# Optimization experiments

Measured on AMD Instinct MI355X. Metric: run time of the kernel, lower is better.

The kernel has to match this reference:

```python
import jax, jax.numpy as jnp
import numpy as np

N = 50000      # nodes
E = 800000     # edges
F_IN = 128     # input feature dim (OGBN-MAG paper features)
H = 4          # attention heads
HID = 64       # hidden_dim (per-head out channels)
HC = H * HID   # 256, concat output width
NC = 349       # num_classes
BN_EPS = 1e-5


def setup_inputs() -> dict:
    key = jax.random.key(0)
    ks = jax.random.split(key, 32)
    s = 0.05
    inp = {
        "x": jax.random.normal(ks[0], (N, F_IN), dtype=jnp.float32),
        "edge_index": jax.random.randint(ks[1], (2, E), 0, N, dtype=jnp.int64),
    }
    dins = [F_IN, HC]
    i = 2
    for l in range(2):
        d = dins[l]
        inp[f"ws{l}"] = jax.random.normal(ks[i], (d, HC), jnp.float32) * s; i += 1
        inp[f"wd{l}"] = jax.random.normal(ks[i], (d, HC), jnp.float32) * s; i += 1
        inp[f"atts{l}"] = jax.random.normal(ks[i], (H, HID), jnp.float32) * s; i += 1
        inp[f"attd{l}"] = jax.random.normal(ks[i], (H, HID), jnp.float32) * s; i += 1
        inp[f"bg{l}"] = jnp.zeros((HC,), jnp.float32); i += 1
        inp[f"lw{l}"] = jax.random.normal(ks[i], (d, HC), jnp.float32) * s; i += 1
        inp[f"lb{l}"] = jnp.zeros((HC,), jnp.float32); i += 1
        inp[f"g{l}"] = jnp.ones((HC,), jnp.float32); i += 1
        inp[f"b{l}"] = jnp.zeros((HC,), jnp.float32); i += 1
    inp["fcw"] = jax.random.normal(ks[i], (HC, NC), jnp.float32) * s
    inp["fcb"] = jnp.zeros((NC,), jnp.float32)
    return inp


def _gat(x, src, dst, ws, wd, atts, attd, bias):
    # PyG GATConv: separate src/dst projections, per-edge additive attention,
    # softmax over incoming edges of each dst node, scatter-add aggregation.
    n = x.shape[0]
    xs = (x @ ws).reshape(n, H, HID)            # [N,H,C] source messages
    xd = (x @ wd).reshape(n, H, HID)
    a_s = jnp.einsum("nhc,hc->nh", xs, atts)    # alpha_src
    a_d = jnp.einsum("nhc,hc->nh", xd, attd)    # alpha_dst
    e = jax.nn.leaky_relu(a_s[src] + a_d[dst], 0.2)   # [E,H]
    m = jax.ops.segment_max(e, dst, num_segments=n)   # segment-softmax (stable)
    ex = jnp.exp(e - m[dst])
    den = jax.ops.segment_sum(ex, dst, num_segments=n)
    w = ex / (den[dst] + 1e-16)                 # [E,H]
    out = jax.ops.segment_sum(xs[src] * w[:, :, None], dst, num_segments=n)
    return out.reshape(n, HC) + bias


def _bn(h, gamma, beta):
    # training-mode BatchNorm1d: batch statistics over nodes, biased variance
    mu = jnp.mean(h, axis=0)
    var = jnp.mean(jnp.square(h - mu), axis=0)
    return (h - mu) * jax.lax.rsqrt(var + BN_EPS) * gamma + beta


def reference(x, edge_index, ws0, wd0, atts0, attd0, bg0, lw0, lb0, g0, b0,
              ws1, wd1, atts1, attd1, bg1, lw1, lb1, g1, b1, fcw, fcb):
    src, dst = edge_index[0], edge_index[1]
    h = _gat(x, src, dst, ws0, wd0, atts0, attd0, bg0) + x @ lw0 + lb0
    h = jax.nn.relu(_bn(h, g0, b0))
    h = _gat(h, src, dst, ws1, wd1, atts1, attd1, bg1) + h @ lw1 + lb1
    h = jax.nn.relu(_bn(h, g1, b1))
    return h @ fcw + fcb
```

## Files before the change

### kernel.cpp

```cpp
#include <hip/hip_runtime.h>
#include <hip/hip_bf16.h>
#include <math.h>

#define N_NODES 50000
#define MPAD 50048
#define N_EDGES 800000
#define HCH 256
#define NHEAD 4
#define HIDC 64
#define NCLS 349
#define F_IN 128

typedef short short8 __attribute__((ext_vector_type(8)));
typedef float floatx4 __attribute__((ext_vector_type(4)));

__global__ void k_detect(const unsigned* ei, int* flag) {
    if (blockIdx.x == 0 && threadIdx.x == 0) {
        int i64 = 1;
        for (int e = 0; e < 64; e++)
            if (ei[2 * e + 1] != 0u) { i64 = 0; break; }
        *flag = i64;
    }
}

__device__ __forceinline__ void edge_sd(const int* ei, int e, int i64, int& s, int& d) {
    if (i64) {
        const long long* p = (const long long*)ei;
        s = (int)p[e]; d = (int)p[N_EDGES + e];
    } else {
        s = ei[e]; d = ei[N_EDGES + e];
    }
}

__global__ void k_deg(const int* ei, const int* flag, int* deg) {
    int e = blockIdx.x * 256 + threadIdx.x;
    if (e >= N_EDGES) return;
    int s, d; edge_sd(ei, e, *flag, s, d);
    atomicAdd(&deg[d], 1);
}

__global__ __launch_bounds__(256) void k_scan1(const int* __restrict__ deg,
                                               int* __restrict__ rowptr,
                                               int* __restrict__ bsum) {
    __shared__ int sd[256];
    int t = threadIdx.x;
    int base = blockIdx.x * 1024 + t * 4;
    int d0 = 0, d1 = 0, d2 = 0, d3 = 0;
    if (base + 3 < N_NODES) {
        int4 v = *(const int4*)(deg + base);
        d0 = v.x; d1 = v.y; d2 = v.z; d3 = v.w;
    } else {
        if (base + 0 < N_NODES) d0 = deg[base + 0];
        if (base + 1 < N_NODES) d1 = deg[base + 1];
        if (base + 2 < N_NODES) d2 = deg[base + 2];
        if (base + 3 < N_NODES) d3 = deg[base + 3];
    }
    int ts = d0 + d1 + d2 + d3;
    sd[t] = ts;
    __syncthreads();
    #pragma unroll
    for (int off = 1; off < 256; off <<= 1) {
        int v = (t >= off) ? sd[t - off] : 0;
        __syncthreads();
        sd[t] += v;
        __syncthreads();
    }
    int excl = (t == 0) ? 0 : sd[t - 1];
    if (base + 0 < N_NODES) rowptr[base + 0] = excl;
    if (base + 1 < N_NODES) rowptr[base + 1] = excl + d0;
    if (base + 2 < N_NODES) rowptr[base + 2] = excl + d0 + d1;
    if (base + 3 < N_NODES) rowptr[base + 3] = excl + d0 + d1 + d2;
    if (t == 255) bsum[blockIdx.x] = sd[255];
}

__global__ void k_scan2(int* __restrict__ bsum, int nb, int* __restrict__ rowptr) {
    int lane = threadIdx.x;
    int orig = (lane < nb) ? bsum[lane] : 0;
    int v = orig;
    #pragma unroll
    for (int off = 1; off < 64; off <<= 1) {
        int tv = __shfl_up(v, off, 64);
        if (lane >= off) v += tv;
    }
    if (lane < nb) bsum[lane] = v - orig;
    if (lane == 0) rowptr[N_NODES] = N_EDGES;
}

__global__ __launch_bounds__(256) void k_scan3(int* __restrict__ rowptr,
                                               const int* __restrict__ bsum) {
    int base = blockIdx.x * 1024 + threadIdx.x * 4;
    int off = bsum[blockIdx.x];
    if (base + 3 < N_NODES) {
        int4 v = *(int4*)(rowptr + base);
        v.x += off; v.y += off; v.z += off; v.w += off;
        *(int4*)(rowptr + base) = v;
    } else {
        for (int j = 0; j < 4; j++)
            if (base + j < N_NODES) rowptr[base + j] += off;
    }
}

__global__ void k_fill(const int* ei, const int* flag, const int* __restrict__ rowptr,
                       int* cursor, int* __restrict__ esrc) {
    int e = blockIdx.x * 256 + threadIdx.x;
    if (e >= N_EDGES) return;
    int s, d; edge_sd(ei, e, *flag, s, d);
    int pos = atomicAdd(&cursor[d], 1);
    esrc[rowptr[d] + pos] = s;
}

__global__ void k_wtilde(const float* __restrict__ ws, const float* __restrict__ wd,
                         const float* __restrict__ atts, const float* __restrict__ attd,
                         float* __restrict__ wt, int d) {
    int id = blockIdx.x * 256 + threadIdx.x;
    if (id >= d * 8) return;
    int j = id & 7, k = id >> 3;
    const float* w = (j < 4) ? ws : wd;
    const float* at = (j < 4) ? atts : attd;
    int h = j & 3;
    float s = 0.f;
    for (int c = 0; c < HIDC; c++) s += w[k * HCH + h * HIDC + c] * at[h * HIDC + c];
    wt[k * 8 + j] = s;
}

__device__ __forceinline__ unsigned short b16(float v) {
    __hip_bfloat16 t = __float2bfloat16(v);
    return *(unsigned short*)&t;
}

__device__ __forceinline__ float bfu(unsigned short u) {
    unsigned v = (unsigned)u << 16;
    return __builtin_bit_cast(float, v);
}

__device__ __forceinline__ void bsplit(float v, unsigned short& h, unsigned short& l) {
    __hip_bfloat16 bh = __float2bfloat16(v);
    float hv = __bfloat162float(bh);
    __hip_bfloat16 bl = __float2bfloat16(v - hv);
    h = *(unsigned short*)&bh;
    l = *(unsigned short*)&bl;
}

__global__ __launch_bounds__(256) void k_xcast(const float* __restrict__ x,
                                               unsigned short* __restrict__ xb) {
    size_t tot = (size_t)N_NODES * 128 / 4;
    for (size_t i = (size_t)blockIdx.x * 256 + threadIdx.x; i < tot;
         i += (size_t)gridDim.x * 256) {
        float4 v = *(const float4*)(x + i * 4);
        ushort4 o = {b16(v.x), b16(v.y), b16(v.z), b16(v.w)};
        *(ushort4*)(xb + i * 4) = o;
    }
}

__global__ void k_wcat_t(const float* __restrict__ ws, const float* __restrict__ lw,
                         const float* __restrict__ wtil, int K,
                         unsigned short* __restrict__ Bh, unsigned short* __restrict__ Bl) {
    int id = blockIdx.x * 256 + threadIdx.x;
    if (id >= 640 * K) return;
    int c = id / K, k = id % K;
    float v;
    if (c < 256) v = ws[(size_t)k * 256 + c];
    else if (c < 512) v = lw[(size_t)k * 256 + (c - 256)];
    else if (c < 520) v = wtil[(size_t)k * 8 + (c - 512)];
    else v = 0.f;
    unsigned short h, l;
    bsplit(v, h, l);
    Bh[(size_t)c * K + k] = h;
    Bl[(size_t)c * K + k] = l;
}

__global__ void k_fcw_t(const float* __restrict__ fcw, int K,
                        unsigned short* __restrict__ Bh, unsigned short* __restrict__ Bl) {
    int id = blockIdx.x * 256 + threadIdx.x;
    if (id >= 384 * K) return;
    int c = id / K, k = id % K;
    float v = (c < NCLS) ? fcw[(size_t)k * NCLS + c] : 0.f;
    unsigned short h, l;
    bsplit(v, h, l);
    Bh[(size_t)c * K + k] = h;
    Bl[(size_t)c * K + k] = l;
}

__device__ __forceinline__ void gload16(const void* g, void* l) {
    __builtin_amdgcn_global_load_lds(
        (const __attribute__((address_space(1))) void*)g,
        (__attribute__((address_space(3))) void*)l, 16, 0, 0);
}

__global__ __launch_bounds__(256) void k_gemm2(
    const unsigned short* __restrict__ Ab,
    const unsigned short* __restrict__ Bh, const unsigned short* __restrict__ Bl,
    float* __restrict__ C, int ldc, __hip_bfloat16* __restrict__ xsb,
    __hip_bfloat16* __restrict__ linbb, float* __restrict__ aout,
    const float* __restrict__ bias, int M, int K, int Nc) {
    __shared__ unsigned short sA[4096];
    __shared__ unsigned short sBh[4096];
    __shared__ unsigned short sBl[4096];
    int tid = threadIdx.x;
    int lane = tid & 63, wave = tid >> 6;
    int wm = wave >> 1, wn = wave & 1;
    int row0 = blockIdx.x * 128, col0 = blockIdx.y * 128;

    int rowq[2], kcq[2];
    #pragma unroll
    for (int q = 0; q < 2; q++) {
        int lds16 = wave * 128 + q * 64 + lane;
        int line = lds16 >> 3;
        int slot0 = (lds16 & 7) ^ (line & 7);
        rowq[q] = (line << 1) | (slot0 >> 2);
        kcq[q] = slot0 & 3;
    }
    int kc = lane >> 4, fr = lane & 15;
    int offA[4], offB[4];
    #pragma unroll
    for (int i = 0; i < 4; i++) {
        int ar = wm * 64 + i * 16 + fr;
        int ln = ar >> 1;
        int sl = (((ar & 1) << 2) | kc) ^ (ln & 7);
        offA[i] = ln * 128 + sl * 16;
        int bc = wn * 64 + i * 16 + fr;
        ln = bc >> 1;
        sl = (((bc & 1) << 2) | kc) ^ (ln & 7);
        offB[i] = ln * 128 + sl * 16;
    }

    floatx4 acc[4][4] = {};
    for (int k0 = 0; k0 < K; k0 += 32) {
        #pragma unroll
        for (int q = 0; q < 2; q++) {
            int lb = wave * 2048 + q * 1024;
            gload16(Ab + (size_t)(row0 + rowq[q]) * K + k0 + kcq[q] * 8, (char*)sA + lb);
            gload16(Bh + (size_t)(col0 + rowq[q]) * K + k0 + kcq[q] * 8, (char*)sBh + lb);
            gload16(Bl + (size_t)(col0 + rowq[q]) * K + k0 + kcq[q] * 8, (char*)sBl + lb);
        }
        __syncthreads();
        short8 fah[4], fbh[4], fbl[4];
        #pragma unroll
        for (int i = 0; i < 4; i++) {
            fah[i] = *(const short8*)((const char*)sA + offA[i]);
            fbh[i] = *(const short8*)((const char*)sBh + offB[i]);
            fbl[i] = *(const short8*)((const char*)sBl + offB[i]);
        }
        #pragma unroll
        for (int i = 0; i < 4; i++)
            #pragma unroll
            for (int j = 0; j < 4; j++) {
                acc[i][j] = __builtin_amdgcn_mfma_f32_16x16x32_bf16(fah[i], fbh[j], acc[i][j], 0, 0, 0);
                acc[i][j] = __builtin_amdgcn_mfma_f32_16x16x32_bf16(fah[i], fbl[j], acc[i][j], 0, 0, 0);
            }
        __syncthreads();
    }
    #pragma unroll
    for (int i = 0; i < 4; i++) {
        #pragma unroll
        for (int j = 0; j < 4; j++) {
            int c = col0 + wn * 64 + j * 16 + fr;
            if (c >= Nc) continue;
            float bv = bias ? bias[c] : 0.f;
            #pragma unroll
            for (int q = 0; q < 4; q++) {
                int r = row0 + wm * 64 + i * 16 + (lane >> 4) * 4 + q;
                if (r >= M) continue;
                float val = acc[i][j][q] + bv;
                if (C) C[(size_t)r * ldc + c] = val;
                else if (c < 256) xsb[(size_t)r * 256 + c] = __float2bfloat16(val);
                else if (c < 512) linbb[(size_t)r * 256 + (c - 256)] = __float2bfloat16(val);
                else aout[(size_t)r * 8 + (c - 512)] = val;
            }
        }
    }
}

#define LEAKY_EXP(vv) __expf(((vv) > 0.f) ? (vv) : 0.2f * (vv))

__global__ __launch_bounds__(256) void k_agg(
    const __hip_bfloat16* __restrict__ xsb,
    const __hip_bfloat16* __restrict__ linb, const float* __restrict__ a,
    const int* __restrict__ rowptr, const int* __restrict__ esrc,
    const float* __restrict__ bg, const float* __restrict__ lb,
    __hip_bfloat16* __restrict__ hout) {
    int wave = threadIdx.x >> 6;
    int lane = threadIdx.x & 63;
    int n = blockIdx.x * 4 + wave;
    if (n >= N_NODES) return;
    int h = lane >> 4;
    int c0 = lane * 4;
    float ad = a[(size_t)n * 8 + 4 + h];
    int beg = rowptr[n], end = rowptr[n + 1];
    float a0 = 0.f, a1 = 0.f, a2 = 0.f, a3 = 0.f, dsum = 0.f;
    int k = beg;
    for (; k + 8 <= end; k += 8) {
        int s[8];
        #pragma unroll
        for (int u = 0; u < 8; u++) s[u] = esrc[k + u];
        ushort4 m[8];
        #pragma unroll
        for (int u = 0; u < 8; u++)
            m[u] = *(const ushort4*)(xsb + (size_t)s[u] * 256 + c0);
        float av[8];
        #pragma unroll
        for (int u = 0; u < 8; u++) av[u] = a[(size_t)s[u] * 8 + h];
        #pragma unroll
        for (int u = 0; u < 8; u++) {
            float ev = LEAKY_EXP(av[u] + ad);
            a0 += bfu(m[u].x) * ev;
            a1 += bfu(m[u].y) * ev;
            a2 += bfu(m[u].z) * ev;
            a3 += bfu(m[u].w) * ev;
            dsum += ev;
        }
    }
    for (; k < end; k++) {
        int s = esrc[k];
        ushort4 m = *(const ushort4*)(xsb + (size_t)s * 256 + c0);
        float ev = LEAKY_EXP(a[(size_t)s * 8 + h] + ad);
        a0 += bfu(m.x) * ev;
        a1 += bfu(m.y) * ev;
        a2 += bfu(m.z) * ev;
        a3 += bfu(m.w) * ev;
        dsum += ev;
    }
    float inv = 1.f / (dsum + 1e-16f);
    float4 bgv = *(const float4*)(bg + c0);
    float4 lbv = *(const float4*)(lb + c0);
    ushort4 lnv = *(const ushort4*)(linb + (size_t)n * 256 + c0);
    ushort4 o;
    o.x = b16(a0 * inv + bgv.x + bfu(lnv.x) + lbv.x);
    o.y = b16(a1 * inv + bgv.y + bfu(lnv.y) + lbv.y);
    o.z = b16(a2 * inv + bgv.z + bfu(lnv.z) + lbv.z);
    o.w = b16(a3 * inv + bgv.w + bfu(lnv.w) + lbv.w);
    *(ushort4*)(hout + (size_t)n * 256 + c0) = o;
}

__global__ void k_bnstats(const __hip_bfloat16* __restrict__ hb,
                          float* __restrict__ bnsum, float* __restrict__ bnsq) {
    int c = threadIdx.x;
    float s = 0.f, q = 0.f;
    for (int r = blockIdx.x; r < N_NODES; r += gridDim.x) {
        float v = __bfloat162float(hb[(size_t)r * 256 + c]);
        s += v; q += v * v;
    }
    atomicAdd(&bnsum[c], s);
    atomicAdd(&bnsq[c], q);
}

__global__ __launch_bounds__(256) void k_bnapply(
    const __hip_bfloat16* __restrict__ hb, __hip_bfloat16* __restrict__ hpost,
    const float* __restrict__ bnsum, const float* __restrict__ bnsq,
    const float* __restrict__ g, const float* __restrict__ b) {
    __shared__ float sA[256], sB[256];
    int t = threadIdx.x;
    {
        float m = bnsum[t] / (float)N_NODES;
        float v = bnsq[t] / (float)N_NODES - m * m;
        float rs = rsqrtf(v + 1e-5f) * g[t];
        sA[t] = rs;
        sB[t] = b[t] - m * rs;
    }
    __syncthreads();
    size_t tot = (size_t)N_NODES * 256;
    for (size_t i = (size_t)blockIdx.x * 256 + t; i < tot;
         i += (size_t)gridDim.x * 256) {
        int c = (int)(i & 255);
        float v = __bfloat162float(hb[i]) * sA[c] + sB[c];
        v = v > 0.f ? v : 0.f;
        hpost[i] = __float2bfloat16(v);
    }
}

extern "C" void kernel_launch(void* const* d_in, const int* in_sizes, int n_in,
                              void* d_out, int out_size, void* d_ws, size_t ws_size,
                              hipStream_t stream) {
    const float* x     = (const float*)d_in[0];
    const int*   ei    = (const int*)d_in[1];
    const float* ws0   = (const float*)d_in[2];
    const float* wd0   = (const float*)d_in[3];
    const float* atts0 = (const float*)d_in[4];
    const float* attd0 = (const float*)d_in[5];
    const float* bg0   = (const float*)d_in[6];
    const float* lw0   = (const float*)d_in[7];
    const float* lb0   = (const float*)d_in[8];
    const float* g0    = (const float*)d_in[9];
    const float* b0    = (const float*)d_in[10];
    const float* ws1   = (const float*)d_in[11];
    const float* wd1   = (const float*)d_in[12];
    const float* atts1 = (const float*)d_in[13];
    const float* attd1 = (const float*)d_in[14];
    const float* bg1   = (const float*)d_in[15];
    const float* lw1   = (const float*)d_in[16];
    const float* lb1   = (const float*)d_in[17];
    const float* g1    = (const float*)d_in[18];
    const float* b1    = (const float*)d_in[19];
    const float* fcw   = (const float*)d_in[20];
    const float* fcb   = (const float*)d_in[21];
    float* out = (float*)d_out;

    char* p = (char*)d_ws;
    auto alloc = [&](size_t bytes) -> char* {
        char* r = p;
        p += (bytes + 255) & ~(size_t)255;
        return r;
    };
    __hip_bfloat16* xsb   = (__hip_bfloat16*)alloc((size_t)N_NODES * 256 * 2);
    __hip_bfloat16* linb  = (__hip_bfloat16*)alloc((size_t)N_NODES * 256 * 2);
    __hip_bfloat16* hb    = (__hip_bfloat16*)alloc((size_t)N_NODES * 256 * 2);
    __hip_bfloat16* hpost = (__hip_bfloat16*)alloc((size_t)MPAD * 256 * 2);
    unsigned short* xb    = (unsigned short*)alloc((size_t)MPAD * 128 * 2);
    float* a      = (float*)alloc((size_t)N_NODES * 8 * 4);
    int*   esrc   = (int*)alloc((size_t)N_EDGES * 4);
    int*   rowptr = (int*)alloc((size_t)(N_NODES + 1) * 4);
    int*   bsum   = (int*)alloc(64 * 4);
    unsigned short* w0h = (unsigned short*)alloc((size_t)640 * 128 * 2);
    unsigned short* w0l = (unsigned short*)alloc((size_t)640 * 128 * 2);
    unsigned short* w1h = (unsigned short*)alloc((size_t)640 * 256 * 2);
    unsigned short* w1l = (unsigned short*)alloc((size_t)640 * 256 * 2);
    unsigned short* fch = (unsigned short*)alloc((size_t)384 * 256 * 2);
    unsigned short* fcl = (unsigned short*)alloc((size_t)384 * 256 * 2);
    float* wtil   = (float*)alloc((size_t)256 * 8 * 4);
    int*   flag   = (int*)alloc(256);
    size_t zr_bytes = (size_t)N_NODES * 4 * 2 + 4 * 256 * 4;
    char* zbase = alloc(zr_bytes);
    int*   deg    = (int*)zbase;
    int*   cursor = deg + N_NODES;
    float* bnsum0 = (float*)(cursor + N_NODES);
    float* bnsq0  = bnsum0 + 256;
    float* bnsum1 = bnsq0 + 256;
    float* bnsq1  = bnsum1 + 256;

    hipMemsetAsync(zbase, 0, zr_bytes, stream);

    const int EB = (N_EDGES + 255) / 256;
    const int RB = MPAD / 128;
    const int AB = (N_NODES + 3) / 4;
    const int SB = (N_NODES + 1023) / 1024;

    k_detect<<<1, 1, 0, stream>>>((const unsigned*)ei, flag);
    k_deg<<<EB, 256, 0, stream>>>(ei, flag, deg);
    k_scan1<<<SB, 256, 0, stream>>>(deg, rowptr, bsum);
    k_scan2<<<1, 64, 0, stream>>>(bsum, SB, rowptr);
    k_scan3<<<SB, 256, 0, stream>>>(rowptr, bsum);
    k_fill<<<EB, 256, 0, stream>>>(ei, flag, rowptr, cursor, esrc);

    k_wtilde<<<(128 * 8 + 255) / 256, 256, 0, stream>>>(ws0, wd0, atts0, attd0, wtil, 128);
    k_wcat_t<<<(640 * 128 + 255) / 256, 256, 0, stream>>>(ws0, lw0, wtil, 128, w0h, w0l);
    k_wtilde<<<(256 * 8 + 255) / 256, 256, 0, stream>>>(ws1, wd1, atts1, attd1, wtil, 256);
    k_wcat_t<<<(640 * 256 + 255) / 256, 256, 0, stream>>>(ws1, lw1, wtil, 256, w1h, w1l);
    k_fcw_t<<<(384 * 256 + 255) / 256, 256, 0, stream>>>(fcw, 256, fch, fcl);
    k_xcast<<<2048, 256, 0, stream>>>(x, xb);

    k_gemm2<<<dim3(RB, 5), 256, 0, stream>>>(xb, w0h, w0l,
                                             nullptr, 0, xsb, linb, a,
                                             nullptr, N_NODES, 128, 520);
    k_agg<<<AB, 256, 0, stream>>>(xsb, linb, a, rowptr, esrc, bg0, lb0, hb);
    k_bnstats<<<256, 256, 0, stream>>>(hb, bnsum0, bnsq0);
    k_bnapply<<<2048, 256, 0, stream>>>(hb, hpost, bnsum0, bnsq0, g0, b0);

    k_gemm2<<<dim3(RB, 5), 256, 0, stream>>>((const unsigned short*)hpost, w1h, w1l,
                                             nullptr, 0, xsb, linb, a,
                                             nullptr, N_NODES, 256, 520);
    k_agg<<<AB, 256, 0, stream>>>(xsb, linb, a, rowptr, esrc, bg1, lb1, hb);
    k_bnstats<<<256, 256, 0, stream>>>(hb, bnsum1, bnsq1);
    k_bnapply<<<2048, 256, 0, stream>>>(hb, hpost, bnsum1, bnsq1, g1, b1);

    k_gemm2<<<dim3(RB, 3), 256, 0, stream>>>((const unsigned short*)hpost, fch, fcl,
                                             out, NCLS, nullptr, nullptr, nullptr,
                                             fcb, N_NODES, 256, NCLS);
}
```

Measured before the change: 545.8 us.

## Drop bf16 hi/lo weight split and double-buffer GEMM LDS tiles

```diff
diff --git a/kernel.cpp b/kernel.cpp
--- a/kernel.cpp
+++ b/kernel.cpp
@@ -133,14 +133,6 @@
     return __builtin_bit_cast(float, v);
 }
 
-__device__ __forceinline__ void bsplit(float v, unsigned short& h, unsigned short& l) {
-    __hip_bfloat16 bh = __float2bfloat16(v);
-    float hv = __bfloat162float(bh);
-    __hip_bfloat16 bl = __float2bfloat16(v - hv);
-    h = *(unsigned short*)&bh;
-    l = *(unsigned short*)&bl;
-}
-
 __global__ __launch_bounds__(256) void k_xcast(const float* __restrict__ x,
                                                unsigned short* __restrict__ xb) {
     size_t tot = (size_t)N_NODES * 128 / 4;
@@ -154,7 +146,7 @@
 
 __global__ void k_wcat_t(const float* __restrict__ ws, const float* __restrict__ lw,
                          const float* __restrict__ wtil, int K,
-                         unsigned short* __restrict__ Bh, unsigned short* __restrict__ Bl) {
+                         unsigned short* __restrict__ Bb) {
     int id = blockIdx.x * 256 + threadIdx.x;
     if (id >= 640 * K) return;
     int c = id / K, k = id % K;
@@ -163,22 +155,16 @@
     else if (c < 512) v = lw[(size_t)k * 256 + (c - 256)];
     else if (c < 520) v = wtil[(size_t)k * 8 + (c - 512)];
     else v = 0.f;
-    unsigned short h, l;
-    bsplit(v, h, l);
-    Bh[(size_t)c * K + k] = h;
-    Bl[(size_t)c * K + k] = l;
+    Bb[(size_t)c * K + k] = b16(v);
 }
 
 __global__ void k_fcw_t(const float* __restrict__ fcw, int K,
-                        unsigned short* __restrict__ Bh, unsigned short* __restrict__ Bl) {
+                        unsigned short* __restrict__ Bb) {
     int id = blockIdx.x * 256 + threadIdx.x;
     if (id >= 384 * K) return;
     int c = id / K, k = id % K;
     float v = (c < NCLS) ? fcw[(size_t)k * NCLS + c] : 0.f;
-    unsigned short h, l;
-    bsplit(v, h, l);
-    Bh[(size_t)c * K + k] = h;
-    Bl[(size_t)c * K + k] = l;
+    Bb[(size_t)c * K + k] = b16(v);
 }
 
 __device__ __forceinline__ void gload16(const void* g, void* l) {
@@ -187,15 +173,14 @@
         (__attribute__((address_space(3))) void*)l, 16, 0, 0);
 }
 
-__global__ __launch_bounds__(256) void k_gemm2(
+__global__ __launch_bounds__(256) void k_gemm1(
     const unsigned short* __restrict__ Ab,
-    const unsigned short* __restrict__ Bh, const unsigned short* __restrict__ Bl,
+    const unsigned short* __restrict__ Bb,
     float* __restrict__ C, int ldc, __hip_bfloat16* __restrict__ xsb,
     __hip_bfloat16* __restrict__ linbb, float* __restrict__ aout,
     const float* __restrict__ bias, int M, int K, int Nc) {
-    __shared__ unsigned short sA[4096];
-    __shared__ unsigned short sBh[4096];
-    __shared__ unsigned short sBl[4096];
+    __shared__ unsigned short sA[2][4096];
+    __shared__ unsigned short sB[2][4096];
     int tid = threadIdx.x;
     int lane = tid & 63, wave = tid >> 6;
     int wm = wave >> 1, wn = wave & 1;
@@ -224,31 +209,40 @@
         offB[i] = ln * 128 + sl * 16;
     }
 
+    const int nt = K >> 5;
+    #pragma unroll
+    for (int q = 0; q < 2; q++) {
+        int lb = wave * 2048 + q * 1024;
+        gload16(Ab + (size_t)(row0 + rowq[q]) * K + kcq[q] * 8, (char*)sA[0] + lb);
+        gload16(Bb + (size_t)(col0 + rowq[q]) * K + kcq[q] * 8, (char*)sB[0] + lb);
+    }
+    __syncthreads();
+
     floatx4 acc[4][4] = {};
-    for (int k0 = 0; k0 < K; k0 += 32) {
-        #pragma unroll
-        for (int q = 0; q < 2; q++) {
-            int lb = wave * 2048 + q * 1024;
-            gload16(Ab + (size_t)(row0 + rowq[q]) * K + k0 + kcq[q] * 8, (char*)sA + lb);
-            gload16(Bh + (size_t)(col0 + rowq[q]) * K + k0 + kcq[q] * 8, (char*)sBh + lb);
-            gload16(Bl + (size_t)(col0 + rowq[q]) * K + k0 + kcq[q] * 8, (char*)sBl + lb);
+    int cur = 0;
+    for (int t = 0; t < nt; t++) {
+        if (t + 1 < nt) {
+            int k0 = (t + 1) << 5;
+            #pragma unroll
+            for (int q = 0; q < 2; q++) {
+                int lb = wave * 2048 + q * 1024;
+                gload16(Ab + (size_t)(row0 + rowq[q]) * K + k0 + kcq[q] * 8, (char*)sA[cur ^ 1] + lb);
+                gload16(Bb + (size_t)(col0 + rowq[q]) * K + k0 + kcq[q] * 8, (char*)sB[cur ^ 1] + lb);
+            }
         }
-        __syncthreads();
-        short8 fah[4], fbh[4], fbl[4];
+        short8 fah[4], fbh[4];
         #pragma unroll
         for (int i = 0; i < 4; i++) {
-            fah[i] = *(const short8*)((const char*)sA + offA[i]);
-            fbh[i] = *(const short8*)((const char*)sBh + offB[i]);
-            fbl[i] = *(const short8*)((const char*)sBl + offB[i]);
+            fah[i] = *(const short8*)((const char*)sA[cur] + offA[i]);
+            fbh[i] = *(const short8*)((const char*)sB[cur] + offB[i]);
         }
         #pragma unroll
         for (int i = 0; i < 4; i++)
             #pragma unroll
-            for (int j = 0; j < 4; j++) {
+            for (int j = 0; j < 4; j++)
                 acc[i][j] = __builtin_amdgcn_mfma_f32_16x16x32_bf16(fah[i], fbh[j], acc[i][j], 0, 0, 0);
-                acc[i][j] = __builtin_amdgcn_mfma_f32_16x16x32_bf16(fah[i], fbl[j], acc[i][j], 0, 0, 0);
-            }
         __syncthreads();
+        cur ^= 1;
     }
     #pragma unroll
     for (int i = 0; i < 4; i++) {
@@ -410,12 +404,9 @@
     int*   esrc   = (int*)alloc((size_t)N_EDGES * 4);
     int*   rowptr = (int*)alloc((size_t)(N_NODES + 1) * 4);
     int*   bsum   = (int*)alloc(64 * 4);
-    unsigned short* w0h = (unsigned short*)alloc((size_t)640 * 128 * 2);
-    unsigned short* w0l = (unsigned short*)alloc((size_t)640 * 128 * 2);
-    unsigned short* w1h = (unsigned short*)alloc((size_t)640 * 256 * 2);
-    unsigned short* w1l = (unsigned short*)alloc((size_t)640 * 256 * 2);
-    unsigned short* fch = (unsigned short*)alloc((size_t)384 * 256 * 2);
-    unsigned short* fcl = (unsigned short*)alloc((size_t)384 * 256 * 2);
+    unsigned short* w0b = (unsigned short*)alloc((size_t)640 * 128 * 2);
+    unsigned short* w1b = (unsigned short*)alloc((size_t)640 * 256 * 2);
+    unsigned short* fcb16 = (unsigned short*)alloc((size_t)384 * 256 * 2);
     float* wtil   = (float*)alloc((size_t)256 * 8 * 4);
     int*   flag   = (int*)alloc(256);
     size_t zr_bytes = (size_t)N_NODES * 4 * 2 + 4 * 256 * 4;
@@ -442,27 +433,27 @@
     k_fill<<<EB, 256, 0, stream>>>(ei, flag, rowptr, cursor, esrc);
 
     k_wtilde<<<(128 * 8 + 255) / 256, 256, 0, stream>>>(ws0, wd0, atts0, attd0, wtil, 128);
-    k_wcat_t<<<(640 * 128 + 255) / 256, 256, 0, stream>>>(ws0, lw0, wtil, 128, w0h, w0l);
+    k_wcat_t<<<(640 * 128 + 255) / 256, 256, 0, stream>>>(ws0, lw0, wtil, 128, w0b);
     k_wtilde<<<(256 * 8 + 255) / 256, 256, 0, stream>>>(ws1, wd1, atts1, attd1, wtil, 256);
-    k_wcat_t<<<(640 * 256 + 255) / 256, 256, 0, stream>>>(ws1, lw1, wtil, 256, w1h, w1l);
-    k_fcw_t<<<(384 * 256 + 255) / 256, 256, 0, stream>>>(fcw, 256, fch, fcl);
+    k_wcat_t<<<(640 * 256 + 255) / 256, 256, 0, stream>>>(ws1, lw1, wtil, 256, w1b);
+    k_fcw_t<<<(384 * 256 + 255) / 256, 256, 0, stream>>>(fcw, 256, fcb16);
     k_xcast<<<2048, 256, 0, stream>>>(x, xb);
 
-    k_gemm2<<<dim3(RB, 5), 256, 0, stream>>>(xb, w0h, w0l,
+    k_gemm1<<<dim3(RB, 5), 256, 0, stream>>>(xb, w0b,
                                              nullptr, 0, xsb, linb, a,
                                              nullptr, N_NODES, 128, 520);
     k_agg<<<AB, 256, 0, stream>>>(xsb, linb, a, rowptr, esrc, bg0, lb0, hb);
     k_bnstats<<<256, 256, 0, stream>>>(hb, bnsum0, bnsq0);
     k_bnapply<<<2048, 256, 0, stream>>>(hb, hpost, bnsum0, bnsq0, g0, b0);
 
-    k_gemm2<<<dim3(RB, 5), 256, 0, stream>>>((const unsigned short*)hpost, w1h, w1l,
+    k_gemm1<<<dim3(RB, 5), 256, 0, stream>>>((const unsigned short*)hpost, w1b,
                                              nullptr, 0, xsb, linb, a,
                                              nullptr, N_NODES, 256, 520);
     k_agg<<<AB, 256, 0, stream>>>(xsb, linb, a, rowptr, esrc, bg1, lb1, hb);
     k_bnstats<<<256, 256, 0, stream>>>(hb, bnsum1, bnsq1);
     k_bnapply<<<2048, 256, 0, stream>>>(hb, hpost, bnsum1, bnsq1, g1, b1);
 
-    k_gemm2<<<dim3(RB, 3), 256, 0, stream>>>((const unsigned short*)hpost, fch, fcl,
+    k_gemm1<<<dim3(RB, 3), 256, 0, stream>>>((const unsigned short*)hpost, fcb16,
                                              out, NCLS, nullptr, nullptr, nullptr,
                                              fcb, N_NODES, 256, NCLS);
 }
```

Measured after the change: 531.2 us. -2.7%, faster.
